# Performance work log

Hardware: AMD Instinct MI355X
Metric: run time of the kernel (lower is better)

## Reference

```python
import jax, jax.numpy as jnp
import numpy as np

D_MODEL = 1024
NUM_HEADS = 16
DILATION_RATE = 4
SEGMENT_SIZE = 512
BATCH = 4
SEQ_LEN = 8192


def setup_inputs() -> dict:
    key = jax.random.key(0)
    k_x, k_wqkv, k_wo = jax.random.split(key, 3)
    x = jax.random.normal(k_x, (BATCH, SEQ_LEN, D_MODEL), dtype=jnp.float32)
    # Per-dilation-branch FlashMHA params (fused QKV proj + out proj), stacked.
    Wqkv = jax.random.normal(k_wqkv, (DILATION_RATE, 3 * D_MODEL, D_MODEL), dtype=jnp.float32) * 0.02
    bqkv = jnp.zeros((DILATION_RATE, 3 * D_MODEL), dtype=jnp.float32)
    Wo = jax.random.normal(k_wo, (DILATION_RATE, D_MODEL, D_MODEL), dtype=jnp.float32) * 0.02
    bo = jnp.zeros((DILATION_RATE, D_MODEL), dtype=jnp.float32)
    return {"x": x, "Wqkv": Wqkv, "bqkv": bqkv, "Wo": Wo, "bo": bo}


def _branch(x, Wqkv_i, bqkv_i, Wo_i, bo_i, offset):
    """One dilation branch: strided gather -> segmented MHA -> scatter back."""
    B, S, D = x.shape
    hd = D // NUM_HEADS
    x_ = x[:, offset::DILATION_RATE, :]                      # [B, S/r, D]
    n_seg = x_.shape[1] // SEGMENT_SIZE
    x_ = x_.reshape(B, n_seg, SEGMENT_SIZE, D)               # [B, n, s, D]
    qkv = jnp.einsum('bnsd,ed->bnse', x_, Wqkv_i) + bqkv_i   # [B, n, s, 3D]
    q, k, v = jnp.split(qkv, 3, axis=-1)
    q = q.reshape(B, n_seg, SEGMENT_SIZE, NUM_HEADS, hd)
    k = k.reshape(B, n_seg, SEGMENT_SIZE, NUM_HEADS, hd)
    v = v.reshape(B, n_seg, SEGMENT_SIZE, NUM_HEADS, hd)
    scores = jnp.einsum('bnqhd,bnkhd->bnhqk', q, k) / jnp.sqrt(jnp.asarray(hd, q.dtype))
    attn = jax.nn.softmax(scores, axis=-1)
    o = jnp.einsum('bnhqk,bnkhd->bnqhd', attn, v).reshape(B, n_seg, SEGMENT_SIZE, D)
    o = jnp.einsum('bnsd,ed->bnse', o, Wo_i) + bo_i          # out projection
    full = jnp.zeros((B, S, D), x.dtype).at[:, offset::DILATION_RATE, :].set(
        o.reshape(B, -1, D))
    return full


def reference(x, Wqkv, bqkv, Wo, bo):
    outs = [
        _branch(x, Wqkv[i], bqkv[i], Wo[i], bo[i], offset=i % DILATION_RATE)
        for i in range(DILATION_RATE)
    ]
    # softmax over uniform logits -> equal weights, kept for faithfulness
    weights = jax.nn.softmax(jnp.full((DILATION_RATE,), 1.0 / DILATION_RATE, dtype=x.dtype))
    out = outs[0] * weights[0]
    for i in range(1, DILATION_RATE):
        out = out + weights[i] * outs[i]
    return out
```

## Files before the change

kernel.cpp:

```cpp
#include <hip/hip_runtime.h>
#include <hip/hip_bf16.h>


typedef __bf16 bf16_t;
typedef __bf16 bf16x8 __attribute__((ext_vector_type(8)));
typedef __bf16 bf16x4 __attribute__((ext_vector_type(4)));
typedef float  f32x4  __attribute__((ext_vector_type(4)));

typedef __attribute__((address_space(1))) void gvoid;
typedef __attribute__((address_space(3))) void lvoid;

__device__ __forceinline__ void gload16(const void* g, void* l) {
  __builtin_amdgcn_global_load_lds((gvoid*)g, (lvoid*)l, 16, 0, 0);
}

#define MFMA16(a, b, c) __builtin_amdgcn_mfma_f32_16x16x32_bf16((a), (b), (c), 0, 0, 0)

#define BARRIER()  asm volatile("s_barrier" ::: "memory")
#define WAITLGKM0() do { asm volatile("s_waitcnt lgkmcnt(0)" ::: "memory"); \
                         __builtin_amdgcn_sched_barrier(0); } while (0)

__global__ void cvt_f32_bf16(const float* __restrict__ in, bf16_t* __restrict__ out, int n) {
  int i = (blockIdx.x * blockDim.x + threadIdx.x) * 8;
  int stride = gridDim.x * blockDim.x * 8;
  for (; i < n; i += stride) {
    float4 u = *(const float4*)(in + i);
    float4 v = *(const float4*)(in + i + 4);
    bf16x8 o;
    o[0] = (bf16_t)u.x; o[1] = (bf16_t)u.y; o[2] = (bf16_t)u.z; o[3] = (bf16_t)u.w;
    o[4] = (bf16_t)v.x; o[5] = (bf16_t)v.y; o[6] = (bf16_t)v.z; o[7] = (bf16_t)v.w;
    *(bf16x8*)(out + i) = o;
  }
}


#define GEMM8_DECLS()                                                          \
  __shared__ bf16_t As[2][2][128][64];                                         \
  __shared__ bf16_t Bs[2][2][128][64];                                         \
  const int tid = threadIdx.x;                                                 \
  const int l = tid & 63, wid = tid >> 6;                                      \
  const int wr = wid >> 2, wc = wid & 3;                                       \
  const int rl = l & 15, rq = l >> 4;                                          \
  const int trow = tid >> 3;                                                   \
  const size_t swcol = ((size_t)((tid & 7) ^ (trow & 7))) << 3;                \
  f32x4 acc[8][4];                                                             \
  _Pragma("unroll") for (int m = 0; m < 8; ++m)                                \
    _Pragma("unroll") for (int n = 0; n < 4; ++n)                              \
      acc[m][n] = (f32x4){0.f, 0.f, 0.f, 0.f};                                 \
  bf16x8 aq[4][2], bq0[2][2], bq1[2][2];

#define LD_AQ(cur, mh)                                                         \
  do {                                                                         \
    _Pragma("unroll") for (int j = 0; j < 4; ++j)                              \
      _Pragma("unroll") for (int kk = 0; kk < 2; ++kk) {                       \
        int R_ = (mh)*64 + j*16 + rl;                                          \
        int C_ = (kk*32 + rq*8) ^ ((rl & 7) << 3);                             \
        aq[j][kk] = *(const bf16x8*)&As[cur][wr][R_][C_];                      \
      }                                                                        \
  } while (0)

#define LD_BQ(cur, nh, dst)                                                    \
  do {                                                                         \
    _Pragma("unroll") for (int i = 0; i < 2; ++i)                              \
      _Pragma("unroll") for (int kk = 0; kk < 2; ++kk) {                       \
        int R_ = (wc & 1)*64 + ((nh)*2 + i)*16 + rl;                           \
        int C_ = (kk*32 + rq*8) ^ ((rl & 7) << 3);                             \
        dst[i][kk] = *(const bf16x8*)&Bs[cur][wc >> 1][R_][C_];                \
      }                                                                        \
  } while (0)

#define MF_Q(mh, nh, B_)                                                       \
  do {                                                                         \
    __builtin_amdgcn_s_setprio(1);                                             \
    _Pragma("unroll") for (int j = 0; j < 4; ++j)                              \
      _Pragma("unroll") for (int i = 0; i < 2; ++i) {                          \
        acc[(mh)*4+j][(nh)*2+i] = MFMA16(aq[j][0], B_[i][0], acc[(mh)*4+j][(nh)*2+i]); \
        acc[(mh)*4+j][(nh)*2+i] = MFMA16(aq[j][1], B_[i][1], acc[(mh)*4+j][(nh)*2+i]); \
      }                                                                        \
    __builtin_amdgcn_s_setprio(0);                                             \
  } while (0)

#define ST_A(k2, half)                                                         \
  do { if ((k2) < 16) {                                                        \
    bf16_t* d_ = &As[(k2) & 1][half][0][0];                                    \
    gload16(aSrc + (size_t)((half)*128) * ARSTRIDE + (size_t)(k2)*64, d_ + tid*8);          \
    gload16(aSrc + (size_t)((half)*128 + 64) * ARSTRIDE + (size_t)(k2)*64, d_ + 4096 + tid*8); } \
  } while (0)

#define ST_B(k2, half)                                                         \
  do { if ((k2) < 16) {                                                        \
    bf16_t* d_ = &Bs[(k2) & 1][half][0][0];                                    \
    gload16(bSrc + (size_t)((half)*128) * 1024 + (size_t)(k2)*64, d_ + tid*8);              \
    gload16(bSrc + (size_t)((half)*128 + 64) * 1024 + (size_t)(k2)*64, d_ + 4096 + tid*8); } \
  } while (0)

#define GEMM8_MAINLOOP()                                                       \
  ST_A(0, 0); ST_A(0, 1); ST_B(0, 0); ST_B(0, 1);                              \
  ST_B(1, 0); ST_B(1, 1); ST_A(1, 0);                                          \
  asm volatile("s_waitcnt vmcnt(6)" ::: "memory");                             \
  BARRIER();                                                                   \
  _Pragma("unroll 2")                                                          \
  for (int kt = 0; kt < 16; ++kt) {                                            \
    const int cur = kt & 1;                                                    \
                                                                      \
    LD_AQ(cur, 0); LD_BQ(cur, 0, bq0);                                         \
    ST_A(kt + 1, 1);                                                           \
    BARRIER(); WAITLGKM0();                                                    \
    MF_Q(0, 0, bq0);                                                           \
    BARRIER();                                                                 \
                                                                      \
    LD_BQ(cur, 1, bq1);                                                        \
    ST_B(kt + 2, 0);                                                           \
    BARRIER(); WAITLGKM0();                                                    \
    MF_Q(0, 1, bq1);                                                           \
    BARRIER();                                                                 \
                                                                      \
    LD_AQ(cur, 1);                                                             \
    ST_B(kt + 2, 1);                                                           \
    BARRIER(); WAITLGKM0();                                                    \
    MF_Q(1, 1, bq1);                                                           \
    BARRIER();                                                                 \
                                                                      \
    ST_A(kt + 2, 0);                                                           \
    if (kt < 14) asm volatile("s_waitcnt vmcnt(6)" ::: "memory");              \
    else         asm volatile("s_waitcnt vmcnt(0)" ::: "memory");              \
    BARRIER();                                                                 \
    MF_Q(1, 0, bq0);                                                           \
    BARRIER();                                                                 \
  }

__launch_bounds__(512, 2)
__global__ void qkv_gemm8(const bf16_t* __restrict__ xb, const bf16_t* __restrict__ wb,
                          const float* __restrict__ bqkv,
                          bf16_t* __restrict__ qbuf, bf16_t* __restrict__ kbuf,
                          bf16_t* __restrict__ vbuf) {
  GEMM8_DECLS();
  const int flat = blockIdx.y * 12 + blockIdx.x;
  const int nb = (flat & 7) * 192 + (flat >> 3);
  const int ntile = nb % 12, mtile = nb / 12;
  const int br = (mtile >> 3) & 3;
  const int b0 = mtile >> 5, seg0 = (mtile >> 1) & 3, s00 = (mtile & 1) * 256;
  const int xrow_base = (b0 << 13) + br + ((seg0 << 9) + s00) * 4;

#define ARSTRIDE 4096
  const bf16_t* aSrc = xb + (size_t)(xrow_base + 4 * trow) * 1024 + swcol;
  const bf16_t* bSrc = wb + ((size_t)br * 3072 + ntile * 256 + trow) * 1024 + swcol;

  GEMM8_MAINLOOP();
#undef ARSTRIDE

  const int part = ntile >> 2;
#pragma unroll
  for (int m = 0; m < 8; ++m) {
    int g = mtile * 256 + wr * 128 + m * 16 + rq * 4;
    int b = g >> 13, rem = g & 8191;
    int seg = (rem >> 9) & 3, s = rem & 511;
    int sb = (b * 4 + br) * 4 + seg;
#pragma unroll
    for (int n = 0; n < 4; ++n) {
      int e = ntile * 256 + wc * 64 + n * 16 + rl;
      float bias = bqkv[br * 3072 + e];
      int ew = e & 1023, h = ew >> 6, dh = ew & 63;
      size_t bh = (size_t)sb * 16 + h;
      if (part == 0) {
#pragma unroll
        for (int r = 0; r < 4; ++r)
          qbuf[(bh * 512 + (s + r)) * 64 + dh] = (bf16_t)((acc[m][n][r] + bias) * 0.125f);
      } else if (part == 1) {
#pragma unroll
        for (int r = 0; r < 4; ++r)
          kbuf[(bh * 512 + (s + r)) * 64 + dh] = (bf16_t)(acc[m][n][r] + bias);
      } else {
        bf16x4 pk;
#pragma unroll
        for (int r = 0; r < 4; ++r) pk[r] = (bf16_t)(acc[m][n][r] + bias);
        *(bf16x4*)&vbuf[(bh * 64 + dh) * 512 + s] = pk;
      }
    }
  }
}

__launch_bounds__(512, 2)
__global__ void proj_gemm8(const bf16_t* __restrict__ ob, const bf16_t* __restrict__ wob,
                           const float* __restrict__ bo, float* __restrict__ out) {
  GEMM8_DECLS();
  const int flat = blockIdx.y * 4 + blockIdx.x;
  const int nb = (flat & 7) * 64 + (flat >> 3);
  const int ntile = nb & 3, mtile = nb >> 2;
  const int br = (mtile >> 3) & 3;

#define ARSTRIDE 1024
  const bf16_t* aSrc = ob + (size_t)(mtile * 256 + trow) * 1024 + swcol;
  const bf16_t* bSrc = wob + ((size_t)br * 1024 + ntile * 256 + trow) * 1024 + swcol;

  GEMM8_MAINLOOP();
#undef ARSTRIDE

#pragma unroll
  for (int m = 0; m < 8; ++m) {
    int g = mtile * 256 + wr * 128 + m * 16 + rq * 4;
    int b = g >> 13, rem = g & 8191;
    int seg = (rem >> 9) & 3, s = rem & 511;
#pragma unroll
    for (int n = 0; n < 4; ++n) {
      int e = ntile * 256 + wc * 64 + n * 16 + rl;
      float bias = bo[br * 1024 + e];
#pragma unroll
      for (int r = 0; r < 4; ++r) {
        int t = br + (((seg << 9) + s + r) << 2);
        out[((size_t)b * 8192 + t) * 1024 + e] = 0.25f * (acc[m][n][r] + bias);
      }
    }
  }
}

__launch_bounds__(256, 4)
__global__ void attn_kernel(const bf16_t* __restrict__ qb, const bf16_t* __restrict__ kb,
                            const bf16_t* __restrict__ vb, bf16_t* __restrict__ ob) {
  __shared__ bf16_t QPs[64][64];
  __shared__ bf16_t Ks[2][64][64];
  __shared__ bf16_t VTs[2][64][64];
  const int tid = threadIdx.x, l = tid & 63, w = tid >> 6;
  const int qblk = blockIdx.x;
  const int bh = blockIdx.y;

  const int srow = tid >> 3;
  const int scol = (((tid & 7) ^ (srow & 7)) << 3);

  const bf16_t* qsrc = qb + (size_t)bh * 32768 + qblk * 4096;
  gload16(qsrc + srow * 64 + scol, &QPs[0][0] + tid * 8);
  gload16(qsrc + 2048 + srow * 64 + scol, &QPs[0][0] + 2048 + tid * 8);

  const bf16_t* kbase = kb + (size_t)bh * 32768;
  const bf16_t* vbase = vb + (size_t)bh * 32768;

  gload16(kbase + srow * 64 + scol, &Ks[0][0][0] + tid * 8);
  gload16(kbase + 2048 + srow * 64 + scol, &Ks[0][0][0] + 2048 + tid * 8);
  gload16(vbase + (size_t)srow * 512 + scol, &VTs[0][0][0] + tid * 8);
  gload16(vbase + (size_t)(srow + 32) * 512 + scol, &VTs[0][0][0] + 2048 + tid * 8);

  float lsum[4];
  f32x4 accO[4];
#pragma unroll
  for (int r = 0; r < 4; ++r) lsum[r] = 0.f;
#pragma unroll
  for (int di = 0; di < 4; ++di) accO[di] = (f32x4){0.f, 0.f, 0.f, 0.f};

  __syncthreads();

  bf16x8 aq[2];
#pragma unroll
  for (int kk = 0; kk < 2; ++kk) {
    int R = w * 16 + (l & 15);
    int C = (kk * 32 + (l >> 4) * 8) ^ ((R & 7) << 3);
    aq[kk] = *(bf16x8*)&QPs[R][C];
  }

  int cur = 0;
  for (int kt = 0; kt < 8; ++kt) {
    if (kt < 7) {
      int nxt = cur ^ 1;
      gload16(kbase + (kt + 1) * 4096 + srow * 64 + scol, &Ks[nxt][0][0] + tid * 8);
      gload16(kbase + (kt + 1) * 4096 + 2048 + srow * 64 + scol, &Ks[nxt][0][0] + 2048 + tid * 8);
      gload16(vbase + (size_t)srow * 512 + (kt + 1) * 64 + scol, &VTs[nxt][0][0] + tid * 8);
      gload16(vbase + (size_t)(srow + 32) * 512 + (kt + 1) * 64 + scol,
              &VTs[nxt][0][0] + 2048 + tid * 8);
    }

    f32x4 sf[4];
#pragma unroll
    for (int ni = 0; ni < 4; ++ni) sf[ni] = (f32x4){0.f, 0.f, 0.f, 0.f};
#pragma unroll
    for (int kk = 0; kk < 2; ++kk) {
#pragma unroll
      for (int ni = 0; ni < 4; ++ni) {
        int R = ni * 16 + (l & 15);
        int C = (kk * 32 + (l >> 4) * 8) ^ ((R & 7) << 3);
        bf16x8 bk = *(bf16x8*)&Ks[cur][R][C];
        sf[ni] = MFMA16(aq[kk], bk, sf[ni]);
      }
    }

#pragma unroll
    for (int ni = 0; ni < 4; ++ni)
#pragma unroll
      for (int r = 0; r < 4; ++r) {
        float p = __expf(sf[ni][r]);
        sf[ni][r] = p;
        lsum[r] += p;
      }

#pragma unroll
    for (int ni = 0; ni < 4; ++ni)
#pragma unroll
      for (int r = 0; r < 4; ++r) {
        int Rp = w * 16 + ((l >> 4) << 2) + r;
        int Cp = (ni * 16 + (l & 15)) ^ ((Rp & 7) << 3);
        QPs[Rp][Cp] = (bf16_t)sf[ni][r];
      }
    __syncthreads();

#pragma unroll
    for (int kk = 0; kk < 2; ++kk) {
      int Rp = w * 16 + (l & 15);
      int Cp = (kk * 32 + (l >> 4) * 8) ^ ((Rp & 7) << 3);
      bf16x8 apv = *(bf16x8*)&QPs[Rp][Cp];
#pragma unroll
      for (int di = 0; di < 4; ++di) {
        int R = di * 16 + (l & 15);
        int C = (kk * 32 + (l >> 4) * 8) ^ ((R & 7) << 3);
        bf16x8 bv = *(bf16x8*)&VTs[cur][R][C];
        accO[di] = MFMA16(apv, bv, accO[di]);
      }
    }
    __syncthreads();
    cur ^= 1;
  }

#pragma unroll
  for (int r = 0; r < 4; ++r) {
#pragma unroll
    for (int off = 1; off < 16; off <<= 1) lsum[r] += __shfl_xor(lsum[r], off);
  }

  const int sb = bh >> 4, h = bh & 15;
#pragma unroll
  for (int r = 0; r < 4; ++r) {
    float inv = 1.f / lsum[r];
    int tok = sb * 512 + qblk * 64 + w * 16 + ((l >> 4) << 2) + r;
#pragma unroll
    for (int di = 0; di < 4; ++di)
      ob[(size_t)tok * 1024 + h * 64 + di * 16 + (l & 15)] = (bf16_t)(accO[di][r] * inv);
  }
}

extern "C" void kernel_launch(void* const* d_in, const int* in_sizes, int n_in,
                              void* d_out, int out_size, void* d_ws, size_t ws_size,
                              hipStream_t stream) {
  const float* x    = (const float*)d_in[0];
  const float* Wqkv = (const float*)d_in[1];
  const float* bqkv = (const float*)d_in[2];
  const float* Wo   = (const float*)d_in[3];
  const float* bo   = (const float*)d_in[4];
  float* out = (float*)d_out;

  const int NX  = 4 * 8192 * 1024;
  const int NWQ = 4 * 3072 * 1024;
  const int NWO = 4 * 1024 * 1024;
  const int NT  = 32768 * 1024;

  bf16_t* xb   = (bf16_t*)d_ws;
  bf16_t* wqb  = xb + NX;
  bf16_t* wob  = wqb + NWQ;
  bf16_t* qbuf = wob + NWO;
  bf16_t* kbuf = qbuf + NT;
  bf16_t* vbuf = kbuf + NT;
  bf16_t* obuf = xb;

  cvt_f32_bf16<<<4096, 256, 0, stream>>>(x, xb, NX);
  cvt_f32_bf16<<<2048, 256, 0, stream>>>(Wqkv, wqb, NWQ);
  cvt_f32_bf16<<<1024, 256, 0, stream>>>(Wo, wob, NWO);

  qkv_gemm8<<<dim3(12, 128), 512, 0, stream>>>(xb, wqb, bqkv, qbuf, kbuf, vbuf);
  attn_kernel<<<dim3(8, 1024), 256, 0, stream>>>(qbuf, kbuf, vbuf, obuf);
  proj_gemm8<<<dim3(4, 128), 512, 0, stream>>>(obuf, wob, bo, out);
}
```

Baseline: 532.3 us.

## Prefetch next A fragments across GEMM k-tiles and remap attention block order

The GEMM main loop is manually unrolled by two with double-buffered A register fragments, so the first A half for the next k-tile is read from LDS during the last MFMA phase of the current tile. This hides LDS read latency at the start of each tile. Separately, the attention kernel remaps its flat block index so that consecutive blocks are spread across XCDs, which is meant to improve L2 locality for K/V shared between query blocks of one head. The extra register arrays raise VGPR pressure and could reduce occupancy under the 512x2 launch bounds.

```diff
diff --git a/kernel.cpp b/kernel.cpp
--- a/kernel.cpp
+++ b/kernel.cpp
@@ -47,15 +47,15 @@
   _Pragma("unroll") for (int m = 0; m < 8; ++m)                                \
     _Pragma("unroll") for (int n = 0; n < 4; ++n)                              \
       acc[m][n] = (f32x4){0.f, 0.f, 0.f, 0.f};                                 \
-  bf16x8 aq[4][2], bq0[2][2], bq1[2][2];
-
-#define LD_AQ(cur, mh)                                                         \
+  bf16x8 aqE[4][2], aqO[4][2], aqB[4][2], bq0[2][2], bq1[2][2];
+
+#define LD_AQ2(cur, mh, dst)                                                   \
   do {                                                                         \
     _Pragma("unroll") for (int j = 0; j < 4; ++j)                              \
       _Pragma("unroll") for (int kk = 0; kk < 2; ++kk) {                       \
         int R_ = (mh)*64 + j*16 + rl;                                          \
         int C_ = (kk*32 + rq*8) ^ ((rl & 7) << 3);                             \
-        aq[j][kk] = *(const bf16x8*)&As[cur][wr][R_][C_];                      \
+        dst[j][kk] = *(const bf16x8*)&As[cur][wr][R_][C_];                     \
       }                                                                        \
   } while (0)
 
@@ -69,13 +69,13 @@
       }                                                                        \
   } while (0)
 
-#define MF_Q(mh, nh, B_)                                                       \
+#define MF_Q2(mh, nh, A_, B_)                                                  \
   do {                                                                         \
     __builtin_amdgcn_s_setprio(1);                                             \
     _Pragma("unroll") for (int j = 0; j < 4; ++j)                              \
       _Pragma("unroll") for (int i = 0; i < 2; ++i) {                          \
-        acc[(mh)*4+j][(nh)*2+i] = MFMA16(aq[j][0], B_[i][0], acc[(mh)*4+j][(nh)*2+i]); \
-        acc[(mh)*4+j][(nh)*2+i] = MFMA16(aq[j][1], B_[i][1], acc[(mh)*4+j][(nh)*2+i]); \
+        acc[(mh)*4+j][(nh)*2+i] = MFMA16(A_[j][0], B_[i][0], acc[(mh)*4+j][(nh)*2+i]); \
+        acc[(mh)*4+j][(nh)*2+i] = MFMA16(A_[j][1], B_[i][1], acc[(mh)*4+j][(nh)*2+i]); \
       }                                                                        \
     __builtin_amdgcn_s_setprio(0);                                             \
   } while (0)
@@ -94,39 +94,44 @@
     gload16(bSrc + (size_t)((half)*128 + 64) * 1024 + (size_t)(k2)*64, d_ + 4096 + tid*8); } \
   } while (0)
 
+#define GEMM8_TILE(kt, AQ_C, AQ_N, CUR, NXT, DO_PF)                            \
+                                                                      \
+  LD_BQ(CUR, 0, bq0);                                                          \
+  ST_A((kt) + 1, 1);                                                           \
+  BARRIER(); WAITLGKM0();                                                      \
+  MF_Q2(0, 0, AQ_C, bq0);                                                      \
+  BARRIER();                                                                   \
+                                                                      \
+  LD_BQ(CUR, 1, bq1);                                                          \
+  ST_B((kt) + 2, 0);                                                           \
+  BARRIER(); WAITLGKM0();                                                      \
+  MF_Q2(0, 1, AQ_C, bq1);                                                      \
+  BARRIER();                                                                   \
+                                                                      \
+  LD_AQ2(CUR, 1, aqB);                                                         \
+  ST_B((kt) + 2, 1);                                                           \
+  BARRIER(); WAITLGKM0();                                                      \
+  MF_Q2(1, 1, aqB, bq1);                                                       \
+  BARRIER();                                                                   \
+                                                                      \
+  ST_A((kt) + 2, 0);                                                           \
+  if ((kt) < 14) asm volatile("s_waitcnt vmcnt(6)" ::: "memory");              \
+  else           asm volatile("s_waitcnt vmcnt(0)" ::: "memory");              \
+  BARRIER();                                                                   \
+  if (DO_PF) { LD_AQ2(NXT, 0, AQ_N); }        \
+  MF_Q2(1, 0, aqB, bq0);                                                       \
+  BARRIER();
+
 #define GEMM8_MAINLOOP()                                                       \
   ST_A(0, 0); ST_A(0, 1); ST_B(0, 0); ST_B(0, 1);                              \
   ST_B(1, 0); ST_B(1, 1); ST_A(1, 0);                                          \
   asm volatile("s_waitcnt vmcnt(6)" ::: "memory");                             \
   BARRIER();                                                                   \
-  _Pragma("unroll 2")                                                          \
-  for (int kt = 0; kt < 16; ++kt) {                                            \
-    const int cur = kt & 1;                                                    \
-                                                                      \
-    LD_AQ(cur, 0); LD_BQ(cur, 0, bq0);                                         \
-    ST_A(kt + 1, 1);                                                           \
-    BARRIER(); WAITLGKM0();                                                    \
-    MF_Q(0, 0, bq0);                                                           \
-    BARRIER();                                                                 \
-                                                                      \
-    LD_BQ(cur, 1, bq1);                                                        \
-    ST_B(kt + 2, 0);                                                           \
-    BARRIER(); WAITLGKM0();                                                    \
-    MF_Q(0, 1, bq1);                                                           \
-    BARRIER();                                                                 \
-                                                                      \
-    LD_AQ(cur, 1);                                                             \
-    ST_B(kt + 2, 1);                                                           \
-    BARRIER(); WAITLGKM0();                                                    \
-    MF_Q(1, 1, bq1);                                                           \
-    BARRIER();                                                                 \
-                                                                      \
-    ST_A(kt + 2, 0);                                                           \
-    if (kt < 14) asm volatile("s_waitcnt vmcnt(6)" ::: "memory");              \
-    else         asm volatile("s_waitcnt vmcnt(0)" ::: "memory");              \
-    BARRIER();                                                                 \
-    MF_Q(1, 0, bq0);                                                           \
-    BARRIER();                                                                 \
+  LD_AQ2(0, 0, aqE);                                                           \
+  for (int kt2 = 0; kt2 < 8; ++kt2) {                                          \
+    const int ktE = kt2 * 2;                                                   \
+    GEMM8_TILE(ktE,     aqE, aqO, 0, 1, 1);                                    \
+    GEMM8_TILE(ktE + 1, aqO, aqE, 1, 0, (kt2 < 7));                            \
   }
 
 __launch_bounds__(512, 2)
@@ -221,8 +226,11 @@
   __shared__ bf16_t Ks[2][64][64];
   __shared__ bf16_t VTs[2][64][64];
   const int tid = threadIdx.x, l = tid & 63, w = tid >> 6;
-  const int qblk = blockIdx.x;
-  const int bh = blockIdx.y;
+
+  const int flat = blockIdx.y * 8 + blockIdx.x;
+  const int nb = (flat & 7) * 1024 + (flat >> 3);
+  const int qblk = nb & 7;
+  const int bh = nb >> 3;
 
   const int srow = tid >> 3;
   const int scol = (((tid & 7) ^ (srow & 7)) << 3);
```

Measured after the change: 526.4 us. About the same (-1.1%).

## Stage QKV GEMM epilogue through LDS for coalesced vector stores; remap attention blocks

Applied to the files above, without the earlier changes.

The QKV projection epilogue now writes the bias-added, scaled tile into shared memory with an XOR swizzle (transposed for V), synchronises, then writes it back to global memory as 16-byte vectors in contiguous rows. This replaces scattered 2-byte stores. The shared-memory buffers are merged into one aliased array so the epilogue can reuse the GEMM staging space. Separately, the attention kernel remaps its block indices so that consecutive blocks are spread across (bh, qblk) in a way meant to improve cache or XCD locality.

```diff
diff --git a/kernel.cpp b/kernel.cpp
--- a/kernel.cpp
+++ b/kernel.cpp
@@ -34,9 +34,12 @@
 }
 
 
+#define As ((bf16_t(*)[2][128][64])SHM)
+#define Bs ((bf16_t(*)[2][128][64])(SHM + 32768))
+#define Cs ((bf16_t(*)[256])SHM)
+
 #define GEMM8_DECLS()                                                          \
-  __shared__ bf16_t As[2][2][128][64];                                         \
-  __shared__ bf16_t Bs[2][2][128][64];                                         \
+  __shared__ __align__(16) bf16_t SHM[65536];                                  \
   const int tid = threadIdx.x;                                                 \
   const int l = tid & 63, wid = tid >> 6;                                      \
   const int wr = wid >> 2, wc = wid & 3;                                       \
@@ -150,32 +153,57 @@
 #undef ARSTRIDE
 
   const int part = ntile >> 2;
+  const int sb = (b0 * 4 + br) * 4 + seg0;
+  const float scale = (part == 0) ? 0.125f : 1.0f;
+
 #pragma unroll
   for (int m = 0; m < 8; ++m) {
-    int g = mtile * 256 + wr * 128 + m * 16 + rq * 4;
-    int b = g >> 13, rem = g & 8191;
-    int seg = (rem >> 9) & 3, s = rem & 511;
-    int sb = (b * 4 + br) * 4 + seg;
+    int t_loc = wr * 128 + m * 16 + rq * 4;
 #pragma unroll
     for (int n = 0; n < 4; ++n) {
-      int e = ntile * 256 + wc * 64 + n * 16 + rl;
-      float bias = bqkv[br * 3072 + e];
-      int ew = e & 1023, h = ew >> 6, dh = ew & 63;
-      size_t bh = (size_t)sb * 16 + h;
-      if (part == 0) {
-#pragma unroll
-        for (int r = 0; r < 4; ++r)
-          qbuf[(bh * 512 + (s + r)) * 64 + dh] = (bf16_t)((acc[m][n][r] + bias) * 0.125f);
-      } else if (part == 1) {
-#pragma unroll
-        for (int r = 0; r < 4; ++r)
-          kbuf[(bh * 512 + (s + r)) * 64 + dh] = (bf16_t)(acc[m][n][r] + bias);
+      int e_loc = wc * 64 + n * 16 + rl;
+      float bias = bqkv[br * 3072 + ntile * 256 + e_loc];
+      if (part != 2) {
+#pragma unroll
+        for (int r = 0; r < 4; ++r) {
+          int t = t_loc + r;
+          Cs[t][e_loc ^ ((t & 7) << 3)] = (bf16_t)((acc[m][n][r] + bias) * scale);
+        }
       } else {
-        bf16x4 pk;
-#pragma unroll
-        for (int r = 0; r < 4; ++r) pk[r] = (bf16_t)(acc[m][n][r] + bias);
-        *(bf16x4*)&vbuf[(bh * 64 + dh) * 512 + s] = pk;
-      }
+#pragma unroll
+        for (int r = 0; r < 4; ++r) {
+          int t = t_loc + r;
+          Cs[e_loc][t ^ ((e_loc & 7) << 3)] = (bf16_t)(acc[m][n][r] + bias);
+        }
+      }
+    }
+  }
+  __syncthreads();
+
+  if (part != 2) {
+    bf16_t* dst0 = (part == 0) ? qbuf : kbuf;
+    const int hbase = (part == 0) ? ntile * 4 : (ntile - 4) * 4;
+    const int lane8 = tid & 7;
+#pragma unroll
+    for (int it = 0; it < 16; ++it) {
+      int R = it * 64 + (tid >> 3);
+      int h2 = R >> 8, t = R & 255;
+      int e_loc = h2 * 64 + lane8 * 8;
+      bf16x8 v = *(const bf16x8*)&Cs[t][e_loc ^ ((t & 7) << 3)];
+      size_t bh = (size_t)sb * 16 + hbase + h2;
+      *(bf16x8*)&dst0[(bh * 512 + s00 + t) * 64 + lane8 * 8] = v;
+    }
+  } else {
+    const int hbase = (ntile - 8) * 4;
+    const int lane32 = tid & 31;
+#pragma unroll
+    for (int it = 0; it < 16; ++it) {
+      int row_e = it * 16 + (tid >> 5);
+      int t0 = lane32 * 8;
+      bf16x8 v = *(const bf16x8*)&Cs[row_e][t0 ^ ((row_e & 7) << 3)];
+      size_t bh = (size_t)sb * 16 + hbase + (row_e >> 6);
+      int dh = row_e & 63;
+      *(bf16x8*)&vbuf[(bh * 64 + dh) * 512 + s00 + t0] = v;
     }
   }
 }
@@ -221,8 +249,11 @@
   __shared__ bf16_t Ks[2][64][64];
   __shared__ bf16_t VTs[2][64][64];
   const int tid = threadIdx.x, l = tid & 63, w = tid >> 6;
-  const int qblk = blockIdx.x;
-  const int bh = blockIdx.y;
+
+  const int flat = blockIdx.y * 8 + blockIdx.x;
+  const int nb = (flat & 7) * 1024 + (flat >> 3);
+  const int qblk = nb & 7;
+  const int bh = nb >> 3;
 
   const int srow = tid >> 3;
   const int scol = (((tid & 7) ^ (srow & 7)) << 3);
```

Result: faster. 493.1 us (-7.4%).
